# Kernel tuning notes

Hardware: AMD Instinct MI355X
Metric: run time of the kernel (lower is better)

The kernel has to match this reference:

```python
import jax, jax.numpy as jnp
import numpy as np
from jax import lax

B = 2048
C = 8
H = W = 14
NP = H * W  # 196
DIM = 192
THETA = 0.7


def _unfold3(z):
    # z: [B, C, H, W] -> patches [B, C, 9, H, W], matching F.unfold(kernel=3, pad=1)
    p = jnp.pad(z, ((0, 0), (0, 0), (1, 1), (1, 1)))
    return jnp.stack([p[:, :, dy:dy + H, dx:dx + W]
                      for dy in range(3) for dx in range(3)], axis=2)


def setup_inputs() -> dict:
    key = jax.random.key(0)
    ks = jax.random.split(key, 10)
    s = 0.1
    return {
        "x": jax.random.normal(ks[0], (B, 1 + NP, DIM), dtype=jnp.float32),
        "W1": jax.random.normal(ks[1], (C, DIM), dtype=jnp.float32) * s,      # linear1 192->8
        "b1": jax.random.normal(ks[2], (C,), dtype=jnp.float32) * s,
        "conv1_w": jax.random.normal(ks[3], (C, C), dtype=jnp.float32) * s,   # 1x1 conv
        "conv1_b": jax.random.normal(ks[4], (C,), dtype=jnp.float32) * s,
        "cdc_w": jax.random.normal(ks[5], (C, C, 1, 5), dtype=jnp.float32) * s,
        "wc1": jax.random.normal(ks[6], (C, C), dtype=jnp.float32) * s,       # WConv1 (1x1)
        "wc2": jax.random.normal(ks[7], (C, C), dtype=jnp.float32) * s,       # WConv2 (1x1)
        "hist_w": jax.random.normal(ks[8], (DIM, C), dtype=jnp.float32) * s,  # linear 8->192
        "hist_b": jax.random.normal(ks[9], (DIM,), dtype=jnp.float32) * s,
    }


def reference(x, W1, b1, conv1_w, conv1_b, cdc_w, wc1, wc2, hist_w, hist_b):
    class_token, tok = x[:, :1, :], x[:, 1:, :]
    # linear1: [B,196,192] -> [B,196,8]
    t = jnp.einsum('bnd,cd->bnc', tok, W1) + b1
    # -> [B,8,14,14]
    t = t.reshape(-1, H, W, C).transpose(0, 3, 1, 2)

    # conv1 (1x1)
    x1 = jnp.einsum('bihw,oi->bohw', t, conv1_w) + conv1_b[None, :, None, None]

    # CDC: scatter the 1x5 weights into a 3x3 cross-shaped kernel
    w5 = cdc_w[:, :, 0, :]  # [O,I,5]
    z = jnp.zeros((C, C, 1), dtype=cdc_w.dtype)
    k9 = jnp.concatenate([z, w5[:, :, 0:1], z,
                          w5[:, :, 1:2], w5[:, :, 2:3], w5[:, :, 3:4],
                          z, w5[:, :, 4:5], z], axis=2).reshape(C, C, 3, 3)
    out_normal = lax.conv_general_dilated(
        t, k9, window_strides=(1, 1), padding=((1, 1), (1, 1)),
        dimension_numbers=('NCHW', 'OIHW', 'NCHW'))
    kernel_diff = cdc_w.sum(axis=(2, 3))  # [O,I]
    out_diff = jnp.einsum('bihw,oi->bohw', t, kernel_diff)
    x2 = out_normal - THETA * out_diff

    z_star = x1 + x2  # [B,8,14,14]

    # TokenHistogram
    mu = jnp.einsum('bihw,oi->bohw', z_star, wc1)
    gamma = jnp.einsum('bihw,oi->bohw', z_star, wc2)
    zp = _unfold3(z_star)   # [B,8,9,14,14]
    mp = _unfold3(mu)
    gp = _unfold3(gamma)
    u = gp * (zp - mp)
    z_hist = jnp.exp(-u * u).sum(axis=2) / 9.0  # [B,8,14,14]
    # torch .reshape(-1, NP, 8): plain row-major reshape (mixes C and HW)
    z_hist = z_hist.reshape(-1, NP, C)
    y = jnp.einsum('bnc,dc->bnd', z_hist, hist_w) + hist_b  # [B,196,192]

    return jnp.concatenate([class_token, y], axis=1)
```

## Files before the change

kernel.cpp:

```cpp
#include <hip/hip_runtime.h>


#define DIMD 192

__launch_bounds__(256, 6)
__global__ void sadapter_kernel(
    const float* __restrict__ x,
    const float* __restrict__ W1,
    const float* __restrict__ b1,
    const float* __restrict__ conv1_w,
    const float* __restrict__ conv1_b,
    const float* __restrict__ cdc_w,
    const float* __restrict__ wc1,
    const float* __restrict__ wc2,
    const float* __restrict__ hist_w,
    const float* __restrict__ hist_b,
    float* __restrict__ out)
{
    __shared__ float smem[6176];
    float* TS    = smem;
    float* HWT   = smem;
    float* HISTB = smem + 1536;
    float* PS    = smem + 2048;
    float* ZH    = smem + 4096;
    float* WB2   = smem + 5664;

    const int tid = threadIdx.x;
    const float* xb   = x   + (size_t)blockIdx.x * (197 * DIMD);
    float*       outb = out + (size_t)blockIdx.x * (197 * DIMD);

    {
        float4 z4 = make_float4(0.f, 0.f, 0.f, 0.f);
        float4 o4 = make_float4(1.f, 1.f, 1.f, 1.f);
        ((float4*)TS)[tid]       = z4;
        ((float4*)TS)[tid + 256] = z4;
        ((float4*)PS)[tid]       = o4;
        ((float4*)PS)[tid + 256] = o4;
    }
    if (tid < 64) {
        const float* c5 = cdc_w + tid * 5;
        float k0 = c5[0], k1 = c5[1], k2 = c5[2], k3 = c5[3], k4 = c5[4];
        float kd = k0 + k1 + k2 + k3 + k4;
        float* wp = WB2 + tid * 8;
        wp[0] = conv1_w[tid] + k2 - 0.7f * kd;
        wp[1] = k0;
        wp[2] = k1;
        wp[3] = k3;
        wp[4] = k4;
        wp[5] = wc1[tid];
        wp[6] = wc2[tid];
        wp[7] = 0.f;
    }
    __syncthreads();

    if (tid < 196) {
        const float4* rowp = (const float4*)(xb + DIMD + tid * DIMD);
        float acc[8];
        #pragma unroll
        for (int c = 0; c < 8; ++c) acc[c] = b1[c];
        #pragma unroll 2
        for (int d8 = 0; d8 < 48; d8 += 8) {
            float4 tv[8];
            #pragma unroll
            for (int u = 0; u < 8; ++u) tv[u] = rowp[d8 + u];
            #pragma unroll
            for (int u = 0; u < 8; ++u) {
                const float* wp = W1 + (d8 + u) * 4;
                #pragma unroll
                for (int c = 0; c < 8; ++c) {
                    acc[c] += tv[u].x * wp[c * DIMD + 0] + tv[u].y * wp[c * DIMD + 1]
                            + tv[u].z * wp[c * DIMD + 2] + tv[u].w * wp[c * DIMD + 3];
                }
            }
        }
        int h = tid / 14, w = tid - h * 14;
        float* tp = TS + (h + 1) * 16 + (w + 1);
        #pragma unroll
        for (int c = 0; c < 8; ++c) tp[c * 256] = acc[c];
    } else if (tid >= 208) {
        ((float4*)outb)[tid - 208] = ((const float4*)xb)[tid - 208];
    }
    __syncthreads();

    if (tid < 196) {
        int h = tid / 14, w = tid - h * 14;
        const float* tp = TS + (h + 1) * 16 + (w + 1);
        float zv[8];
        #pragma unroll
        for (int c = 0; c < 8; ++c) zv[c] = conv1_b[c];
        #pragma unroll
        for (int i = 0; i < 8; ++i) {
            float t0 = tp[i * 256];
            float tu = tp[i * 256 - 16];
            float td = tp[i * 256 + 16];
            float tl = tp[i * 256 - 1];
            float tr = tp[i * 256 + 1];
            #pragma unroll
            for (int c = 0; c < 8; ++c) {
                const float* wp = WB2 + (c * 8 + i) * 8;
                float4 wv = *(const float4*)wp;
                float wd = wp[4];
                zv[c] += wv.x * t0 + wv.y * tu + wv.z * tl + wv.w * tr + wd * td;
            }
        }
        float* pp = PS + (h + 1) * 16 + (w + 1);
        #pragma unroll
        for (int c = 0; c < 8; ++c) {
            float mu = 0.f, ga = 0.f;
            #pragma unroll
            for (int i = 0; i < 8; ++i) {
                const float* wp = WB2 + (c * 8 + i) * 8;
                mu += wp[5] * zv[i];
                ga += wp[6] * zv[i];
            }
            float e = ga * (zv[c] - mu);
            pp[c * 256] = __expf(-e * e);
        }
    }
    __syncthreads();

    if (tid < 196) {
        int h = tid / 14, w = tid - h * 14;
        const float* pb = PS + h * 16 + w;
        #pragma unroll
        for (int c = 0; c < 8; ++c) {
            const float* pr = pb + c * 256;
            float s9 = pr[0] + pr[1] + pr[2]
                     + pr[16] + pr[17] + pr[18]
                     + pr[32] + pr[33] + pr[34];
            ZH[c * 196 + tid] = s9 * (1.f / 9.f);
        }
    } else {
        for (int f = tid - 196; f < 384; f += 60) {
            float4 v = ((const float4*)hist_w)[f];
            int d = f >> 1, c0 = (f & 1) * 4;
            HWT[(c0 + 0) * DIMD + d] = v.x;
            HWT[(c0 + 1) * DIMD + d] = v.y;
            HWT[(c0 + 2) * DIMD + d] = v.z;
            HWT[(c0 + 3) * DIMD + d] = v.w;
        }
        for (int f = tid - 196; f < 48; f += 60)
            ((float4*)HISTB)[f] = ((const float4*)hist_b)[f];
    }
    __syncthreads();

    {
        float4* outy = (float4*)(outb + DIMD);
        int d4 = tid % 48;
        int n2 = tid / 48;
        while (n2 < 196) {
            float4 a = ((const float4*)HISTB)[d4];
            const float* zr = ZH + n2 * 8;
            #pragma unroll
            for (int c2 = 0; c2 < 8; ++c2) {
                float s = zr[c2];
                float4 hv = ((const float4*)(HWT + c2 * DIMD))[d4];
                a.x += s * hv.x; a.y += s * hv.y; a.z += s * hv.z; a.w += s * hv.w;
            }
            outy[n2 * 48 + d4] = a;
            n2 += 5; d4 += 16;
            if (d4 >= 48) { d4 -= 48; n2 += 1; }
        }
    }
}

extern "C" void kernel_launch(void* const* d_in, const int* in_sizes, int n_in,
                              void* d_out, int out_size, void* d_ws, size_t ws_size,
                              hipStream_t stream)
{
    const float* x       = (const float*)d_in[0];
    const float* W1      = (const float*)d_in[1];
    const float* b1      = (const float*)d_in[2];
    const float* conv1_w = (const float*)d_in[3];
    const float* conv1_b = (const float*)d_in[4];
    const float* cdc_w   = (const float*)d_in[5];
    const float* wc1     = (const float*)d_in[6];
    const float* wc2     = (const float*)d_in[7];
    const float* hist_w  = (const float*)d_in[8];
    const float* hist_b  = (const float*)d_in[9];
    float* out = (float*)d_out;

    sadapter_kernel<<<2048, 256, 0, stream>>>(
        x, W1, b1, conv1_w, conv1_b, cdc_w, wc1, wc2, hist_w, hist_b, out);
}
```

Measured before the change: 166.4 us.

## Compute histogram output per token row from global weights, drop staging buffers

Removes the shared-memory staging of hist_w and hist_b, the ZH buffer and one barrier. Each token thread now computes its reshaped 8-value histogram row directly from PS and writes a full 192-wide output row, reading weights through uniform scalar/global loads. Shared memory shrinks so launch bounds are raised to allow more blocks per CU, and the linear1 loop is reordered to iterate by channel with a full unroll. The risk is that per-thread row writes with a stride of 192 floats are poorly coalesced, and 60 threads sit idle in the last phase.

```diff
diff --git a/kernel.cpp b/kernel.cpp
--- a/kernel.cpp
+++ b/kernel.cpp
@@ -3,7 +3,7 @@
 
 #define DIMD 192
 
-__launch_bounds__(256, 6)
+__launch_bounds__(256, 8)
 __global__ void sadapter_kernel(
     const float* __restrict__ x,
     const float* __restrict__ W1,
@@ -17,13 +17,10 @@
     const float* __restrict__ hist_b,
     float* __restrict__ out)
 {
-    __shared__ float smem[6176];
-    float* TS    = smem;
-    float* HWT   = smem;
-    float* HISTB = smem + 1536;
-    float* PS    = smem + 2048;
-    float* ZH    = smem + 4096;
-    float* WB2   = smem + 5664;
+    __shared__ float smem[4608];
+    float* TS  = smem;
+    float* PS  = smem + 2048;
+    float* WB2 = smem + 4096;
 
     const int tid = threadIdx.x;
     const float* xb   = x   + (size_t)blockIdx.x * (197 * DIMD);
@@ -58,18 +55,18 @@
         float acc[8];
         #pragma unroll
         for (int c = 0; c < 8; ++c) acc[c] = b1[c];
-        #pragma unroll 2
-        for (int d8 = 0; d8 < 48; d8 += 8) {
+        #pragma unroll
+        for (int blk = 0; blk < 6; ++blk) {
             float4 tv[8];
             #pragma unroll
-            for (int u = 0; u < 8; ++u) tv[u] = rowp[d8 + u];
+            for (int u = 0; u < 8; ++u) tv[u] = rowp[blk * 8 + u];
             #pragma unroll
-            for (int u = 0; u < 8; ++u) {
-                const float* wp = W1 + (d8 + u) * 4;
+            for (int c = 0; c < 8; ++c) {
+                const float* wrow = W1 + c * DIMD + blk * 32;
                 #pragma unroll
-                for (int c = 0; c < 8; ++c) {
-                    acc[c] += tv[u].x * wp[c * DIMD + 0] + tv[u].y * wp[c * DIMD + 1]
-                            + tv[u].z * wp[c * DIMD + 2] + tv[u].w * wp[c * DIMD + 3];
+                for (int u = 0; u < 8; ++u) {
+                    acc[c] += tv[u].x * wrow[u * 4 + 0] + tv[u].y * wrow[u * 4 + 1]
+                            + tv[u].z * wrow[u * 4 + 2] + tv[u].w * wrow[u * 4 + 3];
                 }
             }
         }
@@ -77,8 +74,9 @@
         float* tp = TS + (h + 1) * 16 + (w + 1);
         #pragma unroll
         for (int c = 0; c < 8; ++c) tp[c * 256] = acc[c];
-    } else if (tid >= 208) {
-        ((float4*)outb)[tid - 208] = ((const float4*)xb)[tid - 208];
+    } else {
+        int f = tid - 196;
+        if (f < 48) ((float4*)outb)[f] = ((const float4*)xb)[f];
     }
     __syncthreads();
 
@@ -120,46 +118,40 @@
     __syncthreads();
 
     if (tid < 196) {
-        int h = tid / 14, w = tid - h * 14;
-        const float* pb = PS + h * 16 + w;
-        #pragma unroll
-        for (int c = 0; c < 8; ++c) {
-            const float* pr = pb + c * 256;
-            float s9 = pr[0] + pr[1] + pr[2]
-                     + pr[16] + pr[17] + pr[18]
-                     + pr[32] + pr[33] + pr[34];
-            ZH[c * 196 + tid] = s9 * (1.f / 9.f);
+        float zr[8];
+        {
+            int f  = tid * 8;
+            int c  = f / 196;
+            int hw = f - c * 196;
+            int h  = hw / 14;
+            int w  = hw - h * 14;
+            #pragma unroll
+            for (int c2 = 0; c2 < 8; ++c2) {
+                const float* pr = PS + c * 256 + h * 16 + w;
+                float s9 = pr[0]  + pr[1]  + pr[2]
+                         + pr[16] + pr[17] + pr[18]
+                         + pr[32] + pr[33] + pr[34];
+                zr[c2] = s9 * (1.f / 9.f);
+                ++w;
+                if (w == 14) { w = 0; ++h; }
+                if (h == 14) { h = 0; ++c; }
+            }
         }
-    } else {
-        for (int f = tid - 196; f < 384; f += 60) {
-            float4 v = ((const float4*)hist_w)[f];
-            int d = f >> 1, c0 = (f & 1) * 4;
-            HWT[(c0 + 0) * DIMD + d] = v.x;
-            HWT[(c0 + 1) * DIMD + d] = v.y;
-            HWT[(c0 + 2) * DIMD + d] = v.z;
-            HWT[(c0 + 3) * DIMD + d] = v.w;
-        }
-        for (int f = tid - 196; f < 48; f += 60)
-            ((float4*)HISTB)[f] = ((const float4*)hist_b)[f];
-    }
-    __syncthreads();
-
-    {
-        float4* outy = (float4*)(outb + DIMD);
-        int d4 = tid % 48;
-        int n2 = tid / 48;
-        while (n2 < 196) {
-            float4 a = ((const float4*)HISTB)[d4];
-            const float* zr = ZH + n2 * 8;
+        float4* oy = (float4*)(outb + DIMD + tid * DIMD);
+        #pragma unroll 2
+        for (int d4 = 0; d4 < 48; ++d4) {
+            const float* hw_ = hist_w + d4 * 32;
+            const float* hb  = hist_b + d4 * 4;
+            float4 a = make_float4(hb[0], hb[1], hb[2], hb[3]);
             #pragma unroll
             for (int c2 = 0; c2 < 8; ++c2) {
                 float s = zr[c2];
-                float4 hv = ((const float4*)(HWT + c2 * DIMD))[d4];
-                a.x += s * hv.x; a.y += s * hv.y; a.z += s * hv.z; a.w += s * hv.w;
+                a.x += s * hw_[0 * 8 + c2];
+                a.y += s * hw_[1 * 8 + c2];
+                a.z += s * hw_[2 * 8 + c2];
+                a.w += s * hw_[3 * 8 + c2];
             }
-            outy[n2 * 48 + d4] = a;
-            n2 += 5; d4 += 16;
-            if (d4 >= 48) { d4 -= 48; n2 += 1; }
+            oy[d4] = a;
         }
     }
 }
```

Measured after the change: 230.0 us. 38.2% more time.
